# Kernel tuning notes

Measured on AMD Instinct MI355X. Metric: run time of the kernel, lower is better.

Reference implementation:

```python
import jax, jax.numpy as jnp
import numpy as np

B, N, D_IN, D_HID = 8, 2048, 512, 512

def setup_inputs() -> dict:
    key = jax.random.key(0)
    k1, k2, k3 = jax.random.split(key, 3)
    inp = jax.random.normal(k1, (B, N, D_IN), dtype=jnp.float32)
    # nn.Linear(input_size, hidden_size): weight [hidden, in], bias [hidden]
    W = jax.random.normal(k2, (D_HID, D_IN), dtype=jnp.float32) * (1.0 / np.sqrt(D_IN))
    b = jax.random.normal(k3, (D_HID,), dtype=jnp.float32) * 0.01
    return {"input": inp, "W": W, "b": b}

def reference(input, W, b):
    # x = fc(input): [B, N, D_HID]
    x = jnp.einsum('bnd,hd->bnh', input, W) + b
    # scores = x @ x^T (NO scale factor, matching the original): [B, N, N]
    scores = jnp.einsum('bnh,bmh->bnm', x, x)
    attn = jax.nn.softmax(scores, axis=2)
    # output = attn @ raw input (V = input, not the projection): [B, N, D_IN]
    output = jnp.einsum('bnm,bmd->bnd', attn, input)
    return output
```

## Files before the change

### kernel.cpp

```cpp
#include <hip/hip_runtime.h>
#include <hip/hip_bf16.h>
#include <stdint.h>

typedef short vbf16x8 __attribute__((ext_vector_type(8)));
typedef float vf32x4 __attribute__((ext_vector_type(4)));
typedef unsigned short u16;

__device__ __forceinline__ float bf2f(u16 u) {
  union { unsigned int i; float f; } v; v.i = ((unsigned int)u) << 16; return v.f;
}
__device__ __forceinline__ u16 f2bf(float f) {
  union { float f; unsigned int i; } v; v.f = f;
  return (u16)((v.i + 0x7fffu + ((v.i >> 16) & 1u)) >> 16);
}
__device__ __forceinline__ void gld16(const void* g, void* l) {
  __builtin_amdgcn_global_load_lds((const __attribute__((address_space(1))) void*)g,
                                   (__attribute__((address_space(3))) void*)l, 16, 0, 0);
}
template<int N> __device__ __forceinline__ void wait_vmcnt() {
  asm volatile("s_waitcnt vmcnt(%0)" :: "n"(N) : "memory");
}
__device__ __forceinline__ vbf16x8 ldsv(const u16* p) { return *(const vbf16x8*)p; }

__global__ __launch_bounds__(256) void k_convw(const float* __restrict__ W, u16* __restrict__ Wb) {
  int i = blockIdx.x * 256 + threadIdx.x;
  float4 x = ((const float4*)W)[i];
  ushort4 h;
  h.x = f2bf(x.x); h.y = f2bf(x.y); h.z = f2bf(x.z); h.w = f2bf(x.w);
  ((ushort4*)Wb)[i] = h;
}

__global__ __launch_bounds__(256) void k_prep(const float* __restrict__ in,
                                              u16* __restrict__ Abf, u16* __restrict__ Vt) {
  __shared__ u16 Ts[64][72];
  const int tid = threadIdx.x;
  const int n0 = blockIdx.x * 64, d0 = blockIdx.y * 64, b = blockIdx.z;
  const float* src = in + ((long long)b * 2048 + n0) * 512 + d0;
#pragma unroll
  for (int j = 0; j < 4; ++j) {
    int chunk = tid + 256 * j;
    int r = chunk >> 4, c = (chunk & 15) * 4;
    float4 x = *(const float4*)(src + (long long)r * 512 + c);
    ushort4 h;
    h.x = f2bf(x.x); h.y = f2bf(x.y); h.z = f2bf(x.z); h.w = f2bf(x.w);
    *(ushort4*)(Abf + ((long long)b * 2048 + n0 + r) * 512 + d0 + c) = h;
    Ts[c + 0][r] = h.x; Ts[c + 1][r] = h.y; Ts[c + 2][r] = h.z; Ts[c + 3][r] = h.w;
  }
  __syncthreads();
#pragma unroll
  for (int j = 0; j < 2; ++j) {
    int chunk = tid + 256 * j;
    int dr = chunk >> 3, c8 = (chunk & 7) * 8;
    vbf16x8 w = *(const vbf16x8*)&Ts[dr][c8];
    *(vbf16x8*)(Vt + ((long long)b * 512 + d0 + dr) * 2048 + n0 + c8) = w;
  }
}

__device__ __forceinline__ void sround(const u16* g, int K, int k0, u16* ldsbuf,
                                       int r, int srow, int scol, int wv) {
  gld16(g + (long long)(r * 64 + srow) * K + k0 + scol, ldsbuf + r * 4096 + wv * 512);
}

template<bool OUTBF, bool BIAS, int MAP>
__global__ __launch_bounds__(512, 2) void k_gemm(const u16* __restrict__ A,
                                                 const u16* __restrict__ Bt,
                                                 const float* __restrict__ bias,
                                                 void* __restrict__ Cout,
                                                 int M, int N, int K,
                                                 long long sA, long long sB, long long sC) {
  __shared__ __align__(16) u16 As[3 * 16384];
  __shared__ __align__(16) u16 Bs[3 * 8192];

  const int tid = threadIdx.x, lane = tid & 63, wv = tid >> 6;
  const int wr = wv >> 2, wc = wv & 3;

  const int lin = blockIdx.x;
  const int xcd = lin & 7, idx = lin >> 3;
  int zb, browi, bcoli;
  if constexpr (MAP == 0) { zb = xcd; browi = idx >> 4; bcoli = idx & 15; }
  else if constexpr (MAP == 1) { zb = 0; browi = xcd * 8 + (idx >> 2); bcoli = idx & 3; }
  else { zb = xcd; browi = idx >> 2; bcoli = idx & 3; }
  const int brow = browi * 256, bcol = bcoli * 128;
  const long long z = zb;

  const u16* gA = A + z * sA + (long long)brow * K;
  const u16* gB = Bt + z * sB + (long long)bcol * K;
  const int NT = K >> 6;

  const int srow = wv * 8 + (lane >> 3);
  const int scol = (((lane & 7) ^ ((lane >> 3) & 7)) << 3);

  const int rd0 = (lane & 15) * 64 + ((((lane >> 4)) ^ (lane & 7)) << 3);
  const int wrb = wr * 8192;
  const int wcb = wc * 2048;

  vf32x4 acc[8][2] = {};
  vbf16x8 afr[4], bfr[2];

  u16 *A0 = As, *A1 = As + 16384, *A2 = As + 32768;
  u16 *B0 = Bs, *B1 = Bs + 8192, *B2 = Bs + 16384;

  sround(gA, K, 0, A0, 0, srow, scol, wv);
  sround(gA, K, 0, A0, 1, srow, scol, wv);
  sround(gA, K, 0, A0, 2, srow, scol, wv);
  sround(gA, K, 0, A0, 3, srow, scol, wv);
  sround(gB, K, 0, B0, 0, srow, scol, wv);
  sround(gB, K, 0, B0, 1, srow, scol, wv);
  sround(gA, K, 64, A1, 0, srow, scol, wv);
  sround(gA, K, 64, A1, 1, srow, scol, wv);
  sround(gA, K, 64, A1, 2, srow, scol, wv);
  sround(gA, K, 64, A1, 3, srow, scol, wv);
  sround(gB, K, 64, B1, 0, srow, scol, wv);
  sround(gB, K, 64, B1, 1, srow, scol, wv);

  for (int t = 0; t < NT; ++t) {
    const int k2 = (t + 2) * 64;
    const bool st = (t + 2 < NT);

    if (t < NT - 1) wait_vmcnt<6>(); else wait_vmcnt<0>();
    __builtin_amdgcn_sched_barrier(0);
    __builtin_amdgcn_s_barrier();
    __builtin_amdgcn_sched_barrier(0);

#pragma unroll
    for (int n = 0; n < 2; ++n) bfr[n] = ldsv(B0 + wcb + n * 1024 + rd0);
#pragma unroll
    for (int i = 0; i < 4; ++i) afr[i] = ldsv(A0 + wrb + i * 1024 + rd0);
    if (st) { sround(gA, K, k2, A2, 0, srow, scol, wv); sround(gA, K, k2, A2, 1, srow, scol, wv); }
    __builtin_amdgcn_s_setprio(1);
#pragma unroll
    for (int i = 0; i < 4; ++i)
#pragma unroll
      for (int n = 0; n < 2; ++n)
        acc[i][n] = __builtin_amdgcn_mfma_f32_16x16x32_bf16(afr[i], bfr[n], acc[i][n], 0, 0, 0);
    __builtin_amdgcn_s_setprio(0);

#pragma unroll
    for (int i = 0; i < 4; ++i) afr[i] = ldsv(A0 + wrb + (4 + i) * 1024 + rd0);
    if (st) sround(gA, K, k2, A2, 2, srow, scol, wv);
    __builtin_amdgcn_s_setprio(1);
#pragma unroll
    for (int i = 0; i < 4; ++i)
#pragma unroll
      for (int n = 0; n < 2; ++n)
        acc[4 + i][n] = __builtin_amdgcn_mfma_f32_16x16x32_bf16(afr[i], bfr[n], acc[4 + i][n], 0, 0, 0);
    __builtin_amdgcn_s_setprio(0);

#pragma unroll
    for (int n = 0; n < 2; ++n) bfr[n] = ldsv(B0 + wcb + n * 1024 + (rd0 ^ 32));
#pragma unroll
    for (int i = 0; i < 4; ++i) afr[i] = ldsv(A0 + wrb + i * 1024 + (rd0 ^ 32));
    if (st) { sround(gA, K, k2, A2, 3, srow, scol, wv); sround(gB, K, k2, B2, 0, srow, scol, wv); }
    __builtin_amdgcn_s_setprio(1);
#pragma unroll
    for (int i = 0; i < 4; ++i)
#pragma unroll
      for (int n = 0; n < 2; ++n)
        acc[i][n] = __builtin_amdgcn_mfma_f32_16x16x32_bf16(afr[i], bfr[n], acc[i][n], 0, 0, 0);
    __builtin_amdgcn_s_setprio(0);

#pragma unroll
    for (int i = 0; i < 4; ++i) afr[i] = ldsv(A0 + wrb + (4 + i) * 1024 + (rd0 ^ 32));
    if (st) sround(gB, K, k2, B2, 1, srow, scol, wv);
    __builtin_amdgcn_s_setprio(1);
#pragma unroll
    for (int i = 0; i < 4; ++i)
#pragma unroll
      for (int n = 0; n < 2; ++n)
        acc[4 + i][n] = __builtin_amdgcn_mfma_f32_16x16x32_bf16(afr[i], bfr[n], acc[4 + i][n], 0, 0, 0);
    __builtin_amdgcn_s_setprio(0);

    u16* ta = A0; A0 = A1; A1 = A2; A2 = ta;
    u16* tb = B0; B0 = B1; B1 = B2; B2 = tb;
  }

  const long long zc = z * sC;
#pragma unroll
  for (int m = 0; m < 8; ++m) {
    const int row0 = brow + wr * 128 + m * 16 + (lane >> 4) * 4;
#pragma unroll
    for (int n = 0; n < 2; ++n) {
      const int col = bcol + wc * 32 + n * 16 + (lane & 15);
      const float bv = BIAS ? bias[col] : 0.0f;
#pragma unroll
      for (int r = 0; r < 4; ++r) {
        const float v = acc[m][n][r] + bv;
        const long long off = zc + (long long)(row0 + r) * N + col;
        if (OUTBF) ((u16*)Cout)[off] = f2bf(v);
        else       ((float*)Cout)[off] = v;
      }
    }
  }
}

__global__ __launch_bounds__(256) void k_softmax(u16* __restrict__ P) {
  const long long row = blockIdx.x;
  u16* p = P + row * 2048;
  const int tid = threadIdx.x, lane = tid & 63, wv = tid >> 6;
  vbf16x8 v = ((const vbf16x8*)p)[tid];
  float f[8];
#pragma unroll
  for (int j = 0; j < 8; ++j) f[j] = bf2f((u16)v[j]);
  float m = f[0];
#pragma unroll
  for (int j = 1; j < 8; ++j) m = fmaxf(m, f[j]);
  for (int o = 1; o < 64; o <<= 1) m = fmaxf(m, __shfl_xor(m, o));
  __shared__ float redm[4], reds[4];
  if (lane == 0) redm[wv] = m;
  __syncthreads();
  m = fmaxf(fmaxf(redm[0], redm[1]), fmaxf(redm[2], redm[3]));
  float s = 0.0f;
#pragma unroll
  for (int j = 0; j < 8; ++j) { f[j] = __expf(f[j] - m); s += f[j]; }
  for (int o = 1; o < 64; o <<= 1) s += __shfl_xor(s, o);
  if (lane == 0) reds[wv] = s;
  __syncthreads();
  const float inv = 1.0f / (reds[0] + reds[1] + reds[2] + reds[3]);
#pragma unroll
  for (int j = 0; j < 8; ++j) v[j] = (short)f2bf(f[j] * inv);
  ((vbf16x8*)p)[tid] = v;
}

extern "C" void kernel_launch(void* const* d_in, const int* in_sizes, int n_in,
                              void* d_out, int out_size, void* d_ws, size_t ws_size,
                              hipStream_t stream) {
  const float* input = (const float*)d_in[0];
  const float* W     = (const float*)d_in[1];
  const float* bias  = (const float*)d_in[2];
  float* out = (float*)d_out;

  char* ws = (char*)d_ws;
  u16* Xbf = (u16*)(ws);
  u16* Vt  = (u16*)(ws + 16777216);
  u16* P   = (u16*)(ws + 2LL * 16777216);
  u16* Abf = (u16*)(ws + 2LL * 16777216);
  u16* Wb  = (u16*)(ws + 3LL * 16777216);

  k_convw<<<256, 256, 0, stream>>>(W, Wb);
  k_prep<<<dim3(32, 8, 8), 256, 0, stream>>>(input, Abf, Vt);
  k_gemm<true, true, 1><<<256, 512, 0, stream>>>(
      Abf, Wb, bias, Xbf, 16384, 512, 512, 0, 0, 0);
  k_gemm<true, false, 0><<<1024, 512, 0, stream>>>(
      Xbf, Xbf, nullptr, P, 2048, 2048, 512,
      2048LL * 512, 2048LL * 512, 2048LL * 2048);
  k_softmax<<<16384, 256, 0, stream>>>(P);
  k_gemm<false, false, 2><<<256, 512, 0, stream>>>(
      P, Vt, nullptr, out, 2048, 512, 2048,
      2048LL * 2048, 512LL * 2048, 2048LL * 512);
}
```

Measured before the change: 125.3 us.

## Add dedicated 256x256-tile GEMM kernel for the X·Xᵀ score computation

```diff
diff --git a/kernel.cpp b/kernel.cpp
--- a/kernel.cpp
+++ b/kernel.cpp
@@ -77,8 +77,7 @@
   const int lin = blockIdx.x;
   const int xcd = lin & 7, idx = lin >> 3;
   int zb, browi, bcoli;
-  if constexpr (MAP == 0) { zb = xcd; browi = idx >> 4; bcoli = idx & 15; }
-  else if constexpr (MAP == 1) { zb = 0; browi = xcd * 8 + (idx >> 2); bcoli = idx & 3; }
+  if constexpr (MAP == 1) { zb = 0; browi = xcd * 8 + (idx >> 2); bcoli = idx & 3; }
   else { zb = xcd; browi = idx >> 2; bcoli = idx & 3; }
   const int brow = browi * 256, bcol = bcoli * 128;
   const long long z = zb;
@@ -89,7 +88,6 @@
 
   const int srow = wv * 8 + (lane >> 3);
   const int scol = (((lane & 7) ^ ((lane >> 3) & 7)) << 3);
-
   const int rd0 = (lane & 15) * 64 + ((((lane >> 4)) ^ (lane & 7)) << 3);
   const int wrb = wr * 8192;
   const int wcb = wc * 2048;
@@ -193,6 +191,103 @@
   }
 }
 
+__device__ __forceinline__ void sr32(const u16* g, int K, int k0, u16* ldsbuf,
+                                     int r, int srow, int scol, int wv) {
+  gld16(g + (long long)(r * 128 + srow) * K + k0 + scol, ldsbuf + r * 4096 + wv * 512);
+}
+
+__global__ __launch_bounds__(512, 2) void k_gemmS(const u16* __restrict__ X,
+                                                  u16* __restrict__ P) {
+  constexpr int K = 512, N = 2048;
+  __shared__ __align__(16) u16 As[3 * 8192];
+  __shared__ __align__(16) u16 Bs[3 * 8192];
+
+  const int tid = threadIdx.x, lane = tid & 63, wv = tid >> 6;
+  const int wr = wv >> 2, wc = wv & 3;
+
+  const int lin = blockIdx.x;
+  const int xcd = lin & 7, idx = lin >> 3;
+  const int brow = (idx >> 3) * 256, bcol = (idx & 7) * 256;
+  const long long z = xcd;
+
+  const u16* gA = X + z * (2048LL * 512) + (long long)brow * K;
+  const u16* gB = X + z * (2048LL * 512) + (long long)bcol * K;
+  const int NT = K >> 5;
+
+  const int srow = wv * 16 + (lane >> 2);
+  const int scol = (((lane & 3) ^ ((lane >> 2) & 3)) << 3);
+
+  const int rd = (lane & 15) * 32 + ((((lane >> 4)) ^ (lane & 3)) << 3);
+  const int wrb = wr * 4096;
+  const int wcb = wc * 2048;
+
+  vf32x4 acc[8][4] = {};
+  vbf16x8 afr[4], bfr[4];
+
+  u16 *A0 = As, *A1 = As + 8192, *A2 = As + 16384;
+  u16 *B0 = Bs, *B1 = Bs + 8192, *B2 = Bs + 16384;
+
+  sr32(gA, K, 0, A0, 0, srow, scol, wv);
+  sr32(gA, K, 0, A0, 1, srow, scol, wv);
+  sr32(gB, K, 0, B0, 0, srow, scol, wv);
+  sr32(gB, K, 0, B0, 1, srow, scol, wv);
+  sr32(gA, K, 32, A1, 0, srow, scol, wv);
+  sr32(gA, K, 32, A1, 1, srow, scol, wv);
+  sr32(gB, K, 32, B1, 0, srow, scol, wv);
+  sr32(gB, K, 32, B1, 1, srow, scol, wv);
+
+  for (int t = 0; t < NT; ++t) {
+    const int k2 = (t + 2) * 32;
+    const bool st = (t + 2 < NT);
+
+    if (t < NT - 1) wait_vmcnt<4>(); else wait_vmcnt<0>();
+    __builtin_amdgcn_sched_barrier(0);
+    __builtin_amdgcn_s_barrier();
+    __builtin_amdgcn_sched_barrier(0);
+
+#pragma unroll
+    for (int n = 0; n < 4; ++n) bfr[n] = ldsv(B0 + wcb + n * 512 + rd);
+#pragma unroll
+    for (int i = 0; i < 4; ++i) afr[i] = ldsv(A0 + wrb + i * 512 + rd);
+    if (st) { sr32(gA, K, k2, A2, 0, srow, scol, wv); sr32(gA, K, k2, A2, 1, srow, scol, wv); }
+    __builtin_amdgcn_s_setprio(1);
+#pragma unroll
+    for (int i = 0; i < 4; ++i)
+#pragma unroll
+      for (int n = 0; n < 4; ++n)
+        acc[i][n] = __builtin_amdgcn_mfma_f32_16x16x32_bf16(afr[i], bfr[n], acc[i][n], 0, 0, 0);
+    __builtin_amdgcn_s_setprio(0);
+
+#pragma unroll
+    for (int i = 0; i < 4; ++i) afr[i] = ldsv(A0 + wrb + (4 + i) * 512 + rd);
+    if (st) { sr32(gB, K, k2, B2, 0, srow, scol, wv); sr32(gB, K, k2, B2, 1, srow, scol, wv); }
+    __builtin_amdgcn_s_setprio(1);
+#pragma unroll
+    for (int i = 0; i < 4; ++i)
+#pragma unroll
+      for (int n = 0; n < 4; ++n)
+        acc[4 + i][n] = __builtin_amdgcn_mfma_f32_16x16x32_bf16(afr[i], bfr[n], acc[4 + i][n], 0, 0, 0);
+    __builtin_amdgcn_s_setprio(0);
+
+    u16* ta = A0; A0 = A1; A1 = A2; A2 = ta;
+    u16* tb = B0; B0 = B1; B1 = B2; B2 = tb;
+  }
+
+  const long long zc = z * (2048LL * 2048);
+#pragma unroll
+  for (int m = 0; m < 8; ++m) {
+    const int row0 = brow + wr * 128 + m * 16 + (lane >> 4) * 4;
+#pragma unroll
+    for (int n = 0; n < 4; ++n) {
+      const int col = bcol + wc * 64 + n * 16 + (lane & 15);
+#pragma unroll
+      for (int r = 0; r < 4; ++r) {
+        P[zc + (long long)(row0 + r) * N + col] = f2bf(acc[m][n][r]);
+      }
+    }
+  }
+}
+
 __global__ __launch_bounds__(256) void k_softmax(u16* __restrict__ P) {
   const long long row = blockIdx.x;
   u16* p = P + row * 2048;
@@ -240,9 +335,7 @@
   k_prep<<<dim3(32, 8, 8), 256, 0, stream>>>(input, Abf, Vt);
   k_gemm<true, true, 1><<<256, 512, 0, stream>>>(
       Abf, Wb, bias, Xbf, 16384, 512, 512, 0, 0, 0);
-  k_gemm<true, false, 0><<<1024, 512, 0, stream>>>(
-      Xbf, Xbf, nullptr, P, 2048, 2048, 512,
-      2048LL * 512, 2048LL * 512, 2048LL * 2048);
+  k_gemmS<<<512, 512, 0, stream>>>(Xbf, P);
   k_softmax<<<16384, 256, 0, stream>>>(P);
   k_gemm<false, false, 2><<<256, 512, 0, stream>>>(
       P, Vt, nullptr, out, 2048, 512, 2048,
```

Result: no change. 123.4 us (-1.5%).
